# Performance work log

Measured on AMD Instinct MI355X. Metric: run time of the kernel, lower is better.

The kernel has to match this reference:

```python
import jax, jax.numpy as jnp
import numpy as np

B, NOTES, T, IN, H, NH = 32, 78, 128, 80, 128, 2  # batch, notes, time steps, input feats, time hidden, note hidden


def setup_inputs() -> dict:
    key = jax.random.key(0)
    ks = jax.random.split(key, 9)
    s = 0.1
    f32 = jnp.float32
    return {
        "x": jax.random.normal(ks[0], (B, NOTES, T, IN), f32),
        # time LSTM params (PyTorch layout: [4H, in], gate order i,f,g,o)
        "Wih_t": (jax.random.normal(ks[1], (4 * H, IN), f32) * s),
        "Whh_t": (jax.random.normal(ks[2], (4 * H, H), f32) * s),
        "bih_t": (jax.random.normal(ks[3], (4 * H,), f32) * s),
        "bhh_t": (jax.random.normal(ks[4], (4 * H,), f32) * s),
        # note LSTM params (hidden size 2)
        "Wih_n": (jax.random.normal(ks[5], (4 * NH, H), f32) * s),
        "Whh_n": (jax.random.normal(ks[6], (4 * NH, NH), f32) * s),
        "bih_n": (jax.random.normal(ks[7], (4 * NH,), f32) * s),
        "bhh_n": (jax.random.normal(ks[8], (4 * NH,), f32) * s),
    }


def _lstm(x, Wih, Whh, bih, bhh):
    # x: [N, L, in] -> all-step hidden states [N, L, H]; zero initial (h, c)
    N = x.shape[0]
    Hh = Whh.shape[1]
    b = bih + bhh

    def step(carry, xt):
        h, c = carry
        g = xt @ Wih.T + h @ Whh.T + b  # [N, 4H]
        i, f, gg, o = jnp.split(g, 4, axis=-1)
        c = jax.nn.sigmoid(f) * c + jax.nn.sigmoid(i) * jnp.tanh(gg)
        h = jax.nn.sigmoid(o) * jnp.tanh(c)
        return (h, c), h

    h0 = jnp.zeros((N, Hh), x.dtype)
    _, hs = jax.lax.scan(step, (h0, h0), x.transpose(1, 0, 2))  # hs: [L, N, H]
    return hs.transpose(1, 0, 2)


def reference(x, Wih_t, Whh_t, bih_t, bhh_t, Wih_n, Whh_n, bih_n, bhh_n):
    Bn = x.shape[0]
    # time LSTM: one sequence per (batch, note) -> batched into N = B*NOTES
    th = _lstm(x.reshape(Bn * NOTES, T, IN), Wih_t, Whh_t, bih_t, bhh_t)
    th = th.reshape(Bn, NOTES, T, H)
    # note LSTM: sequence over the 78-note axis at each time step -> batch B*T
    xn = th.transpose(0, 2, 1, 3).reshape(Bn * T, NOTES, H)
    nh = _lstm(xn, Wih_n, Whh_n, bih_n, bhh_n).reshape(Bn, T, NOTES, NH)
    return nh.reshape(Bn, T, NOTES * NH)  # [B, T, 156]
```

## Files before the change

### kernel.cpp

```cpp
#include <hip/hip_runtime.h>

#define B_     32
#define NOTES_ 78
#define T_     128
#define IN_    80
#define H_     128
#define NSEQ_  (B_*NOTES_)
#define MBLK   16
#define NBLK1  (NSEQ_/MBLK)
#define SEQ2_  (B_*T_)
#define XN8    (NSEQ_*T_*IN_/8)
#define SHSTR  136

typedef __attribute__((ext_vector_type(8))) short short8;
typedef __attribute__((ext_vector_type(4))) float f32x4;

__device__ __forceinline__ unsigned short f2bf(float f) {
    unsigned u; __builtin_memcpy(&u, &f, 4);
    u += 0x7fffu + ((u >> 16) & 1u);
    return (unsigned short)(u >> 16);
}
__device__ __forceinline__ short8 pack8(const float* p) {
    short8 r;
    #pragma unroll
    for (int k = 0; k < 8; ++k) r[k] = (short)f2bf(p[k]);
    return r;
}
__device__ __forceinline__ float rcpf(float x)  { return __builtin_amdgcn_rcpf(x); }
__device__ __forceinline__ float sigm(float x)  { return rcpf(1.f + __expf(-x)); }
__device__ __forceinline__ float tanh_(float x) { return 2.f * rcpf(1.f + __expf(-2.f*x)) - 1.f; }

__global__ __launch_bounds__(256) void xcvt_kernel(
    const float* __restrict__ x, unsigned short* __restrict__ xb)
{
    const int i = blockIdx.x * 256 + threadIdx.x;
    if (i < XN8) {
        const f32x4 a = *(const f32x4*)(x + (size_t)i * 8);
        const f32x4 b = *(const f32x4*)(x + (size_t)i * 8 + 4);
        short8 r;
        #pragma unroll
        for (int k = 0; k < 4; ++k) { r[k] = (short)f2bf(a[k]); r[4+k] = (short)f2bf(b[k]); }
        *(short8*)(xb + (size_t)i * 8) = r;
    }
}

template<bool XB16>
__global__ __launch_bounds__(512)
__attribute__((amdgpu_waves_per_eu(1, 2)))
void time_lstm_kernel(
    const void* __restrict__ xin,
    const float* __restrict__ Wih,
    const float* __restrict__ Whh,
    const float* __restrict__ bih,
    const float* __restrict__ bhh,
    const float* __restrict__ Wn,
    const float* __restrict__ bn1,
    const float* __restrict__ bn2,
    float* __restrict__ Gn)
{
    __shared__ unsigned short sH[2][MBLK * SHSTR];

    const int tid  = threadIdx.x;
    const int wave = tid >> 6, lane = tid & 63;
    const int m16  = lane & 15, quad = lane >> 4;
    const int seq0 = blockIdx.x * MBLK;
    const int j    = wave * 16 + m16;

    for (int i = tid; i < 2 * MBLK * SHSTR; i += 512)
        ((unsigned short*)sH)[i] = 0;

    const short8 zero8 = (short8){0,0,0,0,0,0,0,0};
    short8 wf[4][3], hf[4][4];
    #pragma unroll
    for (int g = 0; g < 4; ++g) {
        const int n = g * H_ + j;
        #pragma unroll
        for (int kt = 0; kt < 3; ++kt) {
            const int k = kt * 32 + quad * 8;
            wf[g][kt] = (k < IN_) ? pack8(Wih + n * IN_ + k) : zero8;
        }
        #pragma unroll
        for (int kt = 0; kt < 4; ++kt)
            hf[g][kt] = pack8(Whh + n * H_ + kt * 32 + quad * 8);
    }

    short8 wn[4];
    #pragma unroll
    for (int kt = 0; kt < 4; ++kt)
        wn[kt] = (m16 < 8) ? pack8(Wn + m16 * H_ + kt * 32 + quad * 8) : zero8;
    const float bns = (m16 < 8) ? (bn1[m16] + bn2[m16]) : 0.f;
    unsigned gbase[4];
    #pragma unroll
    for (int r = 0; r < 4; ++r) {
        const int sq = seq0 + quad * 4 + r;
        const int bb = sq / NOTES_;
        const int nn = sq - bb * NOTES_;
        gbase[r] = ((unsigned)bb * (T_ * NOTES_) + (unsigned)nn) * 8u + (unsigned)m16;
    }

    float bg4[4];
    #pragma unroll
    for (int g = 0; g < 4; ++g) bg4[g] = bih[g * H_ + j] + bhh[g * H_ + j];

    const float* xrf = XB16 ? nullptr
        : ((const float*)xin + (size_t)(seq0 + m16) * T_ * IN_);
    const unsigned short* xrb = XB16
        ? ((const unsigned short*)xin + (size_t)(seq0 + m16) * T_ * IN_) : nullptr;

    short8 ax0, ax1, ax2 = zero8;
    if (XB16) {
        const unsigned short* p = xrb;
        ax0 = *(const short8*)(p + quad * 8);
        ax1 = *(const short8*)(p + 32 + quad * 8);
        if (quad < 2) ax2 = *(const short8*)(p + 64 + quad * 8);
    } else {
        const float* p = xrf;
        ax0 = pack8(p + quad * 8);
        ax1 = pack8(p + 32 + quad * 8);
        if (quad < 2) ax2 = pack8(p + 64 + quad * 8);
    }

    f32x4 accX[4];
    #pragma unroll
    for (int g = 0; g < 4; ++g) {
        accX[g] = (f32x4){bg4[g], bg4[g], bg4[g], bg4[g]};
        accX[g] = __builtin_amdgcn_mfma_f32_16x16x32_bf16(ax0, wf[g][0], accX[g], 0, 0, 0);
        accX[g] = __builtin_amdgcn_mfma_f32_16x16x32_bf16(ax1, wf[g][1], accX[g], 0, 0, 0);
        accX[g] = __builtin_amdgcn_mfma_f32_16x16x32_bf16(ax2, wf[g][2], accX[g], 0, 0, 0);
    }
    if (XB16) {
        const unsigned short* p = xrb + IN_;
        ax0 = *(const short8*)(p + quad * 8);
        ax1 = *(const short8*)(p + 32 + quad * 8);
        if (quad < 2) ax2 = *(const short8*)(p + 64 + quad * 8);
    } else {
        const float* p = xrf + IN_;
        ax0 = pack8(p + quad * 8);
        ax1 = pack8(p + 32 + quad * 8);
        if (quad < 2) ax2 = pack8(p + 64 + quad * 8);
    }

    float cst[4] = {0.f, 0.f, 0.f, 0.f};

    __syncthreads();

    for (int t = 0; t < T_; ++t) {
        const unsigned short* sHr = sH[t & 1];
        unsigned short*       sHw = sH[(t & 1) ^ 1];

        short8 ah[4];
        #pragma unroll
        for (int kt = 0; kt < 4; ++kt)
            ah[kt] = *(const short8*)(sHr + m16 * SHSTR + kt * 32 + quad * 8);

        f32x4 acc[4];
        #pragma unroll
        for (int g = 0; g < 4; ++g) {
            acc[g] = accX[g];
            #pragma unroll
            for (int kt = 0; kt < 4; ++kt)
                acc[g] = __builtin_amdgcn_mfma_f32_16x16x32_bf16(ah[kt], hf[g][kt], acc[g], 0, 0, 0);
        }

        if (t > 0 && wave == ((t - 1) & 7)) {
            f32x4 an = (f32x4){0.f, 0.f, 0.f, 0.f};
            #pragma unroll
            for (int kt = 0; kt < 4; ++kt)
                an = __builtin_amdgcn_mfma_f32_16x16x32_bf16(ah[kt], wn[kt], an, 0, 0, 0);
            if (m16 < 8) {
                #pragma unroll
                for (int r = 0; r < 4; ++r)
                    Gn[gbase[r] + (unsigned)(t - 1) * (NOTES_ * 8)] = an[r] + bns;
            }
        }

        if (t + 1 < T_) {
            #pragma unroll
            for (int g = 0; g < 4; ++g) {
                accX[g] = (f32x4){bg4[g], bg4[g], bg4[g], bg4[g]};
                accX[g] = __builtin_amdgcn_mfma_f32_16x16x32_bf16(ax0, wf[g][0], accX[g], 0, 0, 0);
                accX[g] = __builtin_amdgcn_mfma_f32_16x16x32_bf16(ax1, wf[g][1], accX[g], 0, 0, 0);
                accX[g] = __builtin_amdgcn_mfma_f32_16x16x32_bf16(ax2, wf[g][2], accX[g], 0, 0, 0);
            }
        }

        if (t + 2 < T_) {
            if (XB16) {
                const unsigned short* p = xrb + (t + 2) * IN_;
                ax0 = *(const short8*)(p + quad * 8);
                ax1 = *(const short8*)(p + 32 + quad * 8);
                if (quad < 2) ax2 = *(const short8*)(p + 64 + quad * 8);
            } else {
                const float* p = xrf + (t + 2) * IN_;
                ax0 = pack8(p + quad * 8);
                ax1 = pack8(p + 32 + quad * 8);
                if (quad < 2) ax2 = pack8(p + 64 + quad * 8);
            }
        }

        #pragma unroll
        for (int r = 0; r < 4; ++r) {
            const float cf = sigm(acc[1][r]) * cst[r] + sigm(acc[0][r]) * tanh_(acc[2][r]);
            cst[r] = cf;
            const float h = sigm(acc[3][r]) * tanh_(cf);
            sHw[(quad * 4 + r) * SHSTR + j] = f2bf(h);
        }

        __builtin_amdgcn_sched_barrier(0);
        asm volatile("s_waitcnt lgkmcnt(0)" ::: "memory");
        __builtin_amdgcn_s_barrier();
        __builtin_amdgcn_sched_barrier(0);
    }

    if (wave == ((T_ - 1) & 7)) {
        const unsigned short* sHr = sH[T_ & 1];
        short8 ah[4];
        #pragma unroll
        for (int kt = 0; kt < 4; ++kt)
            ah[kt] = *(const short8*)(sHr + m16 * SHSTR + kt * 32 + quad * 8);
        f32x4 an = (f32x4){0.f, 0.f, 0.f, 0.f};
        #pragma unroll
        for (int kt = 0; kt < 4; ++kt)
            an = __builtin_amdgcn_mfma_f32_16x16x32_bf16(ah[kt], wn[kt], an, 0, 0, 0);
        if (m16 < 8) {
            #pragma unroll
            for (int r = 0; r < 4; ++r)
                Gn[gbase[r] + (unsigned)(T_ - 1) * (NOTES_ * 8)] = an[r] + bns;
        }
    }
}

__global__ __launch_bounds__(64) void note_out_kernel(
    const float* __restrict__ Gn,
    const float* __restrict__ Whh,
    float* __restrict__ out)
{
    const int q = blockIdx.x * 64 + threadIdx.x;
    if (q >= SEQ2_) return;

    float w0[8], w1[8];
    #pragma unroll
    for (int g = 0; g < 8; ++g) { w0[g] = Whh[g * 2]; w1[g] = Whh[g * 2 + 1]; }

    const float* gp = Gn + (size_t)q * (NOTES_ * 8);
    float* op = out + (size_t)q * (NOTES_ * 2);

    float h0 = 0.f, h1 = 0.f, c0 = 0.f, c1 = 0.f;
    f32x4 ga = *(const f32x4*)(gp);
    f32x4 gb = *(const f32x4*)(gp + 4);
    for (int n = 0; n < NOTES_; ++n) {
        f32x4 na, nb;
        if (n + 1 < NOTES_) {
            na = *(const f32x4*)(gp + (n + 1) * 8);
            nb = *(const f32x4*)(gp + (n + 1) * 8 + 4);
        }
        const float i0 = ga[0] + w0[0] * h0 + w1[0] * h1;
        const float i1 = ga[1] + w0[1] * h0 + w1[1] * h1;
        const float f0 = ga[2] + w0[2] * h0 + w1[2] * h1;
        const float f1 = ga[3] + w0[3] * h0 + w1[3] * h1;
        const float g0 = gb[0] + w0[4] * h0 + w1[4] * h1;
        const float g1 = gb[1] + w0[5] * h0 + w1[5] * h1;
        const float o0 = gb[2] + w0[6] * h0 + w1[6] * h1;
        const float o1 = gb[3] + w0[7] * h0 + w1[7] * h1;
        c0 = sigm(f0) * c0 + sigm(i0) * tanh_(g0);
        c1 = sigm(f1) * c1 + sigm(i1) * tanh_(g1);
        h0 = sigm(o0) * tanh_(c0);
        h1 = sigm(o1) * tanh_(c1);
        op[n * 2 + 0] = h0;
        op[n * 2 + 1] = h1;
        ga = na; gb = nb;
    }
}

extern "C" void kernel_launch(void* const* d_in, const int* in_sizes, int n_in,
                              void* d_out, int out_size, void* d_ws, size_t ws_size,
                              hipStream_t stream) {
    const float* x     = (const float*)d_in[0];
    const float* Wih_t = (const float*)d_in[1];
    const float* Whh_t = (const float*)d_in[2];
    const float* bih_t = (const float*)d_in[3];
    const float* bhh_t = (const float*)d_in[4];
    const float* Wih_n = (const float*)d_in[5];
    const float* Whh_n = (const float*)d_in[6];
    const float* bih_n = (const float*)d_in[7];
    const float* bhh_n = (const float*)d_in[8];
    float* out = (float*)d_out;

    const size_t xb_bytes = (size_t)NSEQ_ * T_ * IN_ * 2;
    const size_t gn_bytes = (size_t)SEQ2_ * NOTES_ * 8 * 4;

    if (ws_size >= xb_bytes + gn_bytes) {
        unsigned short* xb = (unsigned short*)d_ws;
        float* Gn = (float*)((char*)d_ws + xb_bytes);
        xcvt_kernel<<<(XN8 + 255) / 256, 256, 0, stream>>>(x, xb);
        time_lstm_kernel<true><<<NBLK1, 512, 0, stream>>>(
            xb, Wih_t, Whh_t, bih_t, bhh_t, Wih_n, bih_n, bhh_n, Gn);
        note_out_kernel<<<SEQ2_ / 64, 64, 0, stream>>>(Gn, Whh_n, out);
    } else {
        float* Gn = (float*)d_ws;
        time_lstm_kernel<false><<<NBLK1, 512, 0, stream>>>(
            x, Wih_t, Whh_t, bih_t, bhh_t, Wih_n, bih_n, bhh_n, Gn);
        note_out_kernel<<<SEQ2_ / 64, 64, 0, stream>>>(Gn, Whh_n, out);
    }
}
```

Measured before the change: 378.4 us.

## Warp-specialize time LSTM: producer waves compute input projection into LDS

The block is split into 8 recurrent waves and 4 producer waves (768 threads). The producer waves compute the next step's input projection x·Wih^T plus bias and write it into double-buffered LDS, while the recurrent waves only do the h·Whh MFMAs and the gate math. The note-projection weights move into LDS, the recurrent MFMAs get raised scheduling priority, and the gate nonlinearities are merged so one reciprocal serves the four sigmoid/tanh terms. This takes register pressure and serial work off the recurrent critical path, at the cost of extra LDS traffic, more threads per block and possibly lower occupancy.

```diff
diff --git a/kernel.cpp b/kernel.cpp
--- a/kernel.cpp
+++ b/kernel.cpp
@@ -11,6 +11,7 @@
 #define SEQ2_  (B_*T_)
 #define XN8    (NSEQ_*T_*IN_/8)
 #define SHSTR  136
+#define SAXSTR 20
 
 typedef __attribute__((ext_vector_type(8))) short short8;
 typedef __attribute__((ext_vector_type(4))) float f32x4;
@@ -28,7 +29,7 @@
 }
 __device__ __forceinline__ float rcpf(float x)  { return __builtin_amdgcn_rcpf(x); }
 __device__ __forceinline__ float sigm(float x)  { return rcpf(1.f + __expf(-x)); }
-__device__ __forceinline__ float tanh_(float x) { return 2.f * rcpf(1.f + __expf(-2.f*x)) - 1.f; }
+__device__ __forceinline__ float tanhr(float x) { return 2.f * rcpf(1.f + __expf(-2.f*x)) - 1.f; }
 
 __global__ __launch_bounds__(256) void xcvt_kernel(
     const float* __restrict__ x, unsigned short* __restrict__ xb)
@@ -44,9 +45,31 @@
     }
 }
 
+
+#define GN_TILE(TM1)                                                                   \
+    if (wave == ((TM1) & 7)) {                                                         \
+        short8 wnk[4];                                                                 \
+        _Pragma("unroll")                                                              \
+        for (int kt = 0; kt < 4; ++kt)                                                 \
+            wnk[kt] = *(const short8*)(sWn + ((kt * 16 + m16) * 4 + quad) * 8);        \
+        f32x4 an = (f32x4){0.f, 0.f, 0.f, 0.f};                                        \
+        _Pragma("unroll")                                                              \
+        for (int kt = 0; kt < 4; ++kt)                                                 \
+            an = __builtin_amdgcn_mfma_f32_16x16x32_bf16(ah[kt], wnk[kt], an, 0, 0, 0);\
+        if (m16 < 8) {                                                                 \
+            _Pragma("unroll")                                                          \
+            for (int r = 0; r < 4; ++r) {                                              \
+                const int sq = seq0 + quad * 4 + r;                                    \
+                const int bb = sq / NOTES_;                                            \
+                const int nn = sq - bb * NOTES_;                                       \
+                Gn[((unsigned)bb * (T_ * NOTES_) + (unsigned)nn) * 8u + (unsigned)m16  \
+                   + (unsigned)(TM1) * (NOTES_ * 8)] = an[r] + bns;                    \
+            }                                                                          \
+        }                                                                              \
+    }
+
 template<bool XB16>
-__global__ __launch_bounds__(512)
-__attribute__((amdgpu_waves_per_eu(1, 2)))
+__global__ __launch_bounds__(768)
 void time_lstm_kernel(
     const void* __restrict__ xin,
     const float* __restrict__ Wih,
@@ -59,173 +82,191 @@
     float* __restrict__ Gn)
 {
     __shared__ unsigned short sH[2][MBLK * SHSTR];
+    __shared__ float sAx[2][512 * SAXSTR];
+    __shared__ unsigned short sWn[4 * 16 * 4 * 8];
 
     const int tid  = threadIdx.x;
     const int wave = tid >> 6, lane = tid & 63;
     const int m16  = lane & 15, quad = lane >> 4;
     const int seq0 = blockIdx.x * MBLK;
-    const int j    = wave * 16 + m16;
-
-    for (int i = tid; i < 2 * MBLK * SHSTR; i += 512)
+
+    for (int i = tid; i < 2 * MBLK * SHSTR; i += 768)
         ((unsigned short*)sH)[i] = 0;
+    for (int i = tid; i < 4 * 16 * 4 * 8; i += 768) {
+        const int e = i & 7, qq = (i >> 3) & 3, m = (i >> 5) & 15, kt = i >> 9;
+        sWn[i] = (m < 8) ? f2bf(Wn[m * H_ + kt * 32 + qq * 8 + e]) : (unsigned short)0;
+    }
 
     const short8 zero8 = (short8){0,0,0,0,0,0,0,0};
-    short8 wf[4][3], hf[4][4];
-    #pragma unroll
-    for (int g = 0; g < 4; ++g) {
-        const int n = g * H_ + j;
-        #pragma unroll
-        for (int kt = 0; kt < 3; ++kt) {
-            const int k = kt * 32 + quad * 8;
-            wf[g][kt] = (k < IN_) ? pack8(Wih + n * IN_ + k) : zero8;
-        }
-        #pragma unroll
-        for (int kt = 0; kt < 4; ++kt)
-            hf[g][kt] = pack8(Whh + n * H_ + kt * 32 + quad * 8);
-    }
-
-    short8 wn[4];
-    #pragma unroll
-    for (int kt = 0; kt < 4; ++kt)
-        wn[kt] = (m16 < 8) ? pack8(Wn + m16 * H_ + kt * 32 + quad * 8) : zero8;
     const float bns = (m16 < 8) ? (bn1[m16] + bn2[m16]) : 0.f;
-    unsigned gbase[4];
-    #pragma unroll
-    for (int r = 0; r < 4; ++r) {
-        const int sq = seq0 + quad * 4 + r;
-        const int bb = sq / NOTES_;
-        const int nn = sq - bb * NOTES_;
-        gbase[r] = ((unsigned)bb * (T_ * NOTES_) + (unsigned)nn) * 8u + (unsigned)m16;
-    }
-
-    float bg4[4];
-    #pragma unroll
-    for (int g = 0; g < 4; ++g) bg4[g] = bih[g * H_ + j] + bhh[g * H_ + j];
-
-    const float* xrf = XB16 ? nullptr
-        : ((const float*)xin + (size_t)(seq0 + m16) * T_ * IN_);
-    const unsigned short* xrb = XB16
-        ? ((const unsigned short*)xin + (size_t)(seq0 + m16) * T_ * IN_) : nullptr;
-
-    short8 ax0, ax1, ax2 = zero8;
-    if (XB16) {
-        const unsigned short* p = xrb;
-        ax0 = *(const short8*)(p + quad * 8);
-        ax1 = *(const short8*)(p + 32 + quad * 8);
-        if (quad < 2) ax2 = *(const short8*)(p + 64 + quad * 8);
-    } else {
-        const float* p = xrf;
-        ax0 = pack8(p + quad * 8);
-        ax1 = pack8(p + 32 + quad * 8);
-        if (quad < 2) ax2 = pack8(p + 64 + quad * 8);
-    }
-
-    f32x4 accX[4];
-    #pragma unroll
-    for (int g = 0; g < 4; ++g) {
-        accX[g] = (f32x4){bg4[g], bg4[g], bg4[g], bg4[g]};
-        accX[g] = __builtin_amdgcn_mfma_f32_16x16x32_bf16(ax0, wf[g][0], accX[g], 0, 0, 0);
-        accX[g] = __builtin_amdgcn_mfma_f32_16x16x32_bf16(ax1, wf[g][1], accX[g], 0, 0, 0);
-        accX[g] = __builtin_amdgcn_mfma_f32_16x16x32_bf16(ax2, wf[g][2], accX[g], 0, 0, 0);
-    }
-    if (XB16) {
-        const unsigned short* p = xrb + IN_;
-        ax0 = *(const short8*)(p + quad * 8);
-        ax1 = *(const short8*)(p + 32 + quad * 8);
-        if (quad < 2) ax2 = *(const short8*)(p + 64 + quad * 8);
-    } else {
-        const float* p = xrf + IN_;
-        ax0 = pack8(p + quad * 8);
-        ax1 = pack8(p + 32 + quad * 8);
-        if (quad < 2) ax2 = pack8(p + 64 + quad * 8);
-    }
-
-    float cst[4] = {0.f, 0.f, 0.f, 0.f};
-
-    __syncthreads();
-
-    for (int t = 0; t < T_; ++t) {
-        const unsigned short* sHr = sH[t & 1];
-        unsigned short*       sHw = sH[(t & 1) ^ 1];
-
-        short8 ah[4];
-        #pragma unroll
-        for (int kt = 0; kt < 4; ++kt)
-            ah[kt] = *(const short8*)(sHr + m16 * SHSTR + kt * 32 + quad * 8);
-
-        f32x4 acc[4];
+
+    if (wave < 8) {
+        const int j = wave * 16 + m16;
+
+        short8 hf[4][4];
         #pragma unroll
         for (int g = 0; g < 4; ++g) {
-            acc[g] = accX[g];
+            const int n = g * H_ + j;
             #pragma unroll
             for (int kt = 0; kt < 4; ++kt)
-                acc[g] = __builtin_amdgcn_mfma_f32_16x16x32_bf16(ah[kt], hf[g][kt], acc[g], 0, 0, 0);
-        }
-
-        if (t > 0 && wave == ((t - 1) & 7)) {
-            f32x4 an = (f32x4){0.f, 0.f, 0.f, 0.f};
+                hf[g][kt] = pack8(Whh + n * H_ + kt * 32 + quad * 8);
+        }
+        float cst[4] = {0.f, 0.f, 0.f, 0.f};
+
+        __syncthreads();
+
+        for (int t = 0; t < T_; ++t) {
+            const unsigned short* sHr = sH[t & 1];
+            unsigned short*       sHw = sH[(t & 1) ^ 1];
+            const float*          axr = sAx[t & 1];
+
+            short8 ah[4];
             #pragma unroll
             for (int kt = 0; kt < 4; ++kt)
-                an = __builtin_amdgcn_mfma_f32_16x16x32_bf16(ah[kt], wn[kt], an, 0, 0, 0);
-            if (m16 < 8) {
+                ah[kt] = *(const short8*)(sHr + m16 * SHSTR + kt * 32 + quad * 8);
+
+            f32x4 acc[4];
+            #pragma unroll
+            for (int g = 0; g < 4; ++g)
+                acc[g] = *(const f32x4*)(axr + (g * H_ + j) * SAXSTR + quad * 4);
+            __builtin_amdgcn_s_setprio(1);
+            #pragma unroll
+            for (int g = 0; g < 4; ++g) {
                 #pragma unroll
-                for (int r = 0; r < 4; ++r)
-                    Gn[gbase[r] + (unsigned)(t - 1) * (NOTES_ * 8)] = an[r] + bns;
-            }
-        }
-
-        if (t + 1 < T_) {
-            #pragma unroll
-            for (int g = 0; g < 4; ++g) {
-                accX[g] = (f32x4){bg4[g], bg4[g], bg4[g], bg4[g]};
-                accX[g] = __builtin_amdgcn_mfma_f32_16x16x32_bf16(ax0, wf[g][0], accX[g], 0, 0, 0);
-                accX[g] = __builtin_amdgcn_mfma_f32_16x16x32_bf16(ax1, wf[g][1], accX[g], 0, 0, 0);
-                accX[g] = __builtin_amdgcn_mfma_f32_16x16x32_bf16(ax2, wf[g][2], accX[g], 0, 0, 0);
-            }
-        }
-
-        if (t + 2 < T_) {
-            if (XB16) {
-                const unsigned short* p = xrb + (t + 2) * IN_;
-                ax0 = *(const short8*)(p + quad * 8);
-                ax1 = *(const short8*)(p + 32 + quad * 8);
-                if (quad < 2) ax2 = *(const short8*)(p + 64 + quad * 8);
-            } else {
-                const float* p = xrf + (t + 2) * IN_;
-                ax0 = pack8(p + quad * 8);
-                ax1 = pack8(p + 32 + quad * 8);
-                if (quad < 2) ax2 = pack8(p + 64 + quad * 8);
-            }
-        }
-
+                for (int kt = 0; kt < 4; ++kt)
+                    acc[g] = __builtin_amdgcn_mfma_f32_16x16x32_bf16(ah[kt], hf[g][kt], acc[g], 0, 0, 0);
+            }
+            __builtin_amdgcn_s_setprio(0);
+
+            if (t > 0) GN_TILE(t - 1)
+
+            float ei[4], ef[4], eg[4], eo[4];
+            #pragma unroll
+            for (int r = 0; r < 4; ++r) {
+                ei[r] = __expf(-acc[0][r]);
+                ef[r] = __expf(-acc[1][r]);
+                eg[r] = __expf(-2.f * acc[2][r]);
+                eo[r] = __expf(-acc[3][r]);
+            }
+            #pragma unroll
+            for (int r = 0; r < 4; ++r) {
+                const float di = 1.f + ei[r], df = 1.f + ef[r];
+                const float dg = 1.f + eg[r], dd = 1.f + eo[r];
+                const float s1 = di * df, s2 = dg * dd;
+                const float R  = rcpf(s1 * s2);
+                const float Rs2 = R * s2, Rs1 = R * s1;
+                const float si = Rs2 * df;
+                const float sf = Rs2 * di;
+                const float so = Rs1 * dg;
+                const float tg = 2.f * (Rs1 * dd) - 1.f;
+                const float cf = sf * cst[r] + si * tg;
+                cst[r] = cf;
+                const float h = so * tanhr(cf);
+                sHw[(quad * 4 + r) * SHSTR + j] = f2bf(h);
+            }
+
+            __builtin_amdgcn_sched_barrier(0);
+            asm volatile("s_waitcnt lgkmcnt(0)" ::: "memory");
+            __builtin_amdgcn_s_barrier();
+            __builtin_amdgcn_sched_barrier(0);
+        }
+
+        {
+            const unsigned short* sHr = sH[T_ & 1];
+            short8 ah[4];
+            #pragma unroll
+            for (int kt = 0; kt < 4; ++kt)
+                ah[kt] = *(const short8*)(sHr + m16 * SHSTR + kt * 32 + quad * 8);
+            GN_TILE(T_ - 1)
+        }
+    } else {
+        const int u = wave - 8;
+
+        short8 wfh[8][3];
+        float  bg8[8];
         #pragma unroll
-        for (int r = 0; r < 4; ++r) {
-            const float cf = sigm(acc[1][r]) * cst[r] + sigm(acc[0][r]) * tanh_(acc[2][r]);
-            cst[r] = cf;
-            const float h = sigm(acc[3][r]) * tanh_(cf);
-            sHw[(quad * 4 + r) * SHSTR + j] = f2bf(h);
-        }
-
-        __builtin_amdgcn_sched_barrier(0);
-        asm volatile("s_waitcnt lgkmcnt(0)" ::: "memory");
-        __builtin_amdgcn_s_barrier();
-        __builtin_amdgcn_sched_barrier(0);
-    }
-
-    if (wave == ((T_ - 1) & 7)) {
-        const unsigned short* sHr = sH[T_ & 1];
-        short8 ah[4];
-        #pragma unroll
-        for (int kt = 0; kt < 4; ++kt)
-            ah[kt] = *(const short8*)(sHr + m16 * SHSTR + kt * 32 + quad * 8);
-        f32x4 an = (f32x4){0.f, 0.f, 0.f, 0.f};
-        #pragma unroll
-        for (int kt = 0; kt < 4; ++kt)
-            an = __builtin_amdgcn_mfma_f32_16x16x32_bf16(ah[kt], wn[kt], an, 0, 0, 0);
-        if (m16 < 8) {
-            #pragma unroll
-            for (int r = 0; r < 4; ++r)
-                Gn[gbase[r] + (unsigned)(T_ - 1) * (NOTES_ * 8)] = an[r] + bns;
+        for (int nt = 0; nt < 8; ++nt) {
+            const int n = u * H_ + nt * 16 + m16;
+            #pragma unroll
+            for (int kt = 0; kt < 3; ++kt) {
+                const int k = kt * 32 + quad * 8;
+                wfh[nt][kt] = (k < IN_) ? pack8(Wih + n * IN_ + k) : zero8;
+            }
+            bg8[nt] = bih[n] + bhh[n];
+        }
+
+        const float* xrf = XB16 ? nullptr
+            : ((const float*)xin + (size_t)(seq0 + m16) * T_ * IN_);
+        const unsigned short* xrb = XB16
+            ? ((const unsigned short*)xin + (size_t)(seq0 + m16) * T_ * IN_) : nullptr;
+
+        short8 ax0, ax1, ax2 = zero8;
+        if (XB16) {
+            const unsigned short* p = xrb;
+            ax0 = *(const short8*)(p + quad * 8);
+            ax1 = *(const short8*)(p + 32 + quad * 8);
+            if (quad < 2) ax2 = *(const short8*)(p + 64 + quad * 8);
+        } else {
+            const float* p = xrf;
+            ax0 = pack8(p + quad * 8);
+            ax1 = pack8(p + 32 + quad * 8);
+            if (quad < 2) ax2 = pack8(p + 64 + quad * 8);
+        }
+        {
+            float* wp = sAx[0];
+            #pragma unroll
+            for (int nt = 0; nt < 8; ++nt) {
+                f32x4 a8 = (f32x4){bg8[nt], bg8[nt], bg8[nt], bg8[nt]};
+                a8 = __builtin_amdgcn_mfma_f32_16x16x32_bf16(ax0, wfh[nt][0], a8, 0, 0, 0);
+                a8 = __builtin_amdgcn_mfma_f32_16x16x32_bf16(ax1, wfh[nt][1], a8, 0, 0, 0);
+                a8 = __builtin_amdgcn_mfma_f32_16x16x32_bf16(ax2, wfh[nt][2], a8, 0, 0, 0);
+                *(f32x4*)(wp + (u * H_ + nt * 16 + m16) * SAXSTR + quad * 4) = a8;
+            }
+        }
+        if (XB16) {
+            const unsigned short* p = xrb + IN_;
+            ax0 = *(const short8*)(p + quad * 8);
+            ax1 = *(const short8*)(p + 32 + quad * 8);
+            if (quad < 2) ax2 = *(const short8*)(p + 64 + quad * 8);
+        } else {
+            const float* p = xrf + IN_;
+            ax0 = pack8(p + quad * 8);
+            ax1 = pack8(p + 32 + quad * 8);
+            if (quad < 2) ax2 = pack8(p + 64 + quad * 8);
+        }
+
+        __syncthreads();
+
+        for (int t = 0; t < T_; ++t) {
+            if (t + 1 < T_) {
+                float* wp = sAx[(t + 1) & 1];
+                #pragma unroll
+                for (int nt = 0; nt < 8; ++nt) {
+                    f32x4 a8 = (f32x4){bg8[nt], bg8[nt], bg8[nt], bg8[nt]};
+                    a8 = __builtin_amdgcn_mfma_f32_16x16x32_bf16(ax0, wfh[nt][0], a8, 0, 0, 0);
+                    a8 = __builtin_amdgcn_mfma_f32_16x16x32_bf16(ax1, wfh[nt][1], a8, 0, 0, 0);
+                    a8 = __builtin_amdgcn_mfma_f32_16x16x32_bf16(ax2, wfh[nt][2], a8, 0, 0, 0);
+                    *(f32x4*)(wp + (u * H_ + nt * 16 + m16) * SAXSTR + quad * 4) = a8;
+                }
+            }
+            if (t + 2 < T_) {
+                if (XB16) {
+                    const unsigned short* p = xrb + (t + 2) * IN_;
+                    ax0 = *(const short8*)(p + quad * 8);
+                    ax1 = *(const short8*)(p + 32 + quad * 8);
+                    if (quad < 2) ax2 = *(const short8*)(p + 64 + quad * 8);
+                } else {
+                    const float* p = xrf + (t + 2) * IN_;
+                    ax0 = pack8(p + quad * 8);
+                    ax1 = pack8(p + 32 + quad * 8);
+                    if (quad < 2) ax2 = pack8(p + 64 + quad * 8);
+                }
+            }
+
+            __builtin_amdgcn_sched_barrier(0);
+            asm volatile("s_waitcnt lgkmcnt(0)" ::: "memory");
+            __builtin_amdgcn_s_barrier();
+            __builtin_amdgcn_sched_barrier(0);
         }
     }
 }
@@ -262,10 +303,10 @@
         const float g1 = gb[1] + w0[5] * h0 + w1[5] * h1;
         const float o0 = gb[2] + w0[6] * h0 + w1[6] * h1;
         const float o1 = gb[3] + w0[7] * h0 + w1[7] * h1;
-        c0 = sigm(f0) * c0 + sigm(i0) * tanh_(g0);
-        c1 = sigm(f1) * c1 + sigm(i1) * tanh_(g1);
-        h0 = sigm(o0) * tanh_(c0);
-        h1 = sigm(o1) * tanh_(c1);
+        c0 = sigm(f0) * c0 + sigm(i0) * tanhr(g0);
+        c1 = sigm(f1) * c1 + sigm(i1) * tanhr(g1);
+        h0 = sigm(o0) * tanhr(c0);
+        h1 = sigm(o1) * tanhr(c1);
         op[n * 2 + 0] = h0;
         op[n * 2 + 1] = h1;
         ga = na; gb = nb;
@@ -293,12 +334,12 @@
         unsigned short* xb = (unsigned short*)d_ws;
         float* Gn = (float*)((char*)d_ws + xb_bytes);
         xcvt_kernel<<<(XN8 + 255) / 256, 256, 0, stream>>>(x, xb);
-        time_lstm_kernel<true><<<NBLK1, 512, 0, stream>>>(
+        time_lstm_kernel<true><<<NBLK1, 768, 0, stream>>>(
             xb, Wih_t, Whh_t, bih_t, bhh_t, Wih_n, bih_n, bhh_n, Gn);
         note_out_kernel<<<SEQ2_ / 64, 64, 0, stream>>>(Gn, Whh_n, out);
     } else {
         float* Gn = (float*)d_ws;
-        time_lstm_kernel<false><<<NBLK1, 512, 0, stream>>>(
+        time_lstm_kernel<false><<<NBLK1, 768, 0, stream>>>(
             x, Wih_t, Whh_t, bih_t, bhh_t, Wih_n, bih_n, bhh_n, Gn);
         note_out_kernel<<<SEQ2_ / 64, 64, 0, stream>>>(Gn, Whh_n, out);
     }
```

Measured after the change: 354.3 us. 1.07x faster.
